# Performance work log

Measured on AMD Instinct MI355X. Metric: run time of the kernel, lower is better.

## Reference

```python
import jax, jax.numpy as jnp
import numpy as np

B, L, D, H = 8, 1024, 1024, 16
K = D // H

def setup_inputs() -> dict:
    key = jax.random.key(0)
    k1, k2, k3 = jax.random.split(key, 3)
    scale = 1.0 / np.sqrt(D)
    return {
        "x": jax.random.normal(k1, (B, L, D), dtype=jnp.float32),
        "w_in": jax.random.normal(k2, (D, 3 * D), dtype=jnp.float32) * scale,
        "b_in": jnp.zeros((3 * D,), dtype=jnp.float32),
        "w_out": jax.random.normal(k3, (D, D), dtype=jnp.float32) * scale,
        "b_out": jnp.zeros((D,), dtype=jnp.float32),
    }

def reference(x, w_in, b_in, w_out, b_out):
    # Fused QKV projection: [B, L, 3D]
    qkv = x @ w_in + b_in
    q, k, v = jnp.split(qkv, 3, axis=-1)
    # [B, L, D] -> [B, H, L, K]
    def to_heads(t):
        return t.reshape(B, L, H, K).transpose(0, 2, 1, 3)
    q, k, v = to_heads(q), to_heads(k), to_heads(v)
    # Full [B, H, L, L] score matrix (non-flash, as in source)
    logits = jnp.einsum('bhlk,bhmk->bhlm', q, k) / jnp.sqrt(jnp.float32(K))
    # NOTE: the source computes softmax but then (bug, reproduced faithfully)
    # uses the raw logits in the value contraction. causal_mask defaults False.
    out = jnp.einsum('bhlm,bhmk->bhlk', logits, v)
    out = out.transpose(0, 2, 1, 3).reshape(B, L, D)
    return out @ w_out + b_out
```

## Files before the change

### kernel.cpp

```cpp
#include <hip/hip_runtime.h>
#include <hip/hip_bf16.h>


typedef __attribute__((ext_vector_type(8))) short short8;
typedef __attribute__((ext_vector_type(4))) float f32x4;

static __device__ __forceinline__ short f2bf(float f) {
  __hip_bfloat16 h = __float2bfloat16(f);
  return __builtin_bit_cast(short, h);
}
static __device__ __forceinline__ float bf2f(short s) {
  unsigned int u = ((unsigned int)(unsigned short)s) << 16;
  return __builtin_bit_cast(float, u);
}

#define GLOAD16(src, dst)                                        \
  __builtin_amdgcn_global_load_lds(                              \
      (const __attribute__((address_space(1))) void*)(src),      \
      (__attribute__((address_space(3))) void*)(dst), 16, 0, 0)

__global__ __launch_bounds__(256) void cast_f32_bf16_kernel(
    const float* __restrict__ in, __hip_bfloat16* __restrict__ out) {
  size_t i = ((size_t)blockIdx.x * 256 + threadIdx.x) * 8;
  float4 v0 = *(const float4*)(in + i);
  float4 v1 = *(const float4*)(in + i + 4);
  short8 o;
  o[0] = f2bf(v0.x); o[1] = f2bf(v0.y); o[2] = f2bf(v0.z); o[3] = f2bf(v0.w);
  o[4] = f2bf(v1.x); o[5] = f2bf(v1.y); o[6] = f2bf(v1.z); o[7] = f2bf(v1.w);
  *(short8*)((__hip_bfloat16*)out + i) = o;
}

__global__ __launch_bounds__(256) void transpose_cast_kernel(
    const float* __restrict__ in, __hip_bfloat16* __restrict__ out, int R, int C) {
  __shared__ float tile[32][33];
  int c0 = blockIdx.x * 32, r0 = blockIdx.y * 32;
  int tx = threadIdx.x & 31;
  int ty = threadIdx.x >> 5;
#pragma unroll
  for (int i = 0; i < 4; ++i)
    tile[ty + i * 8][tx] = in[(size_t)(r0 + ty + i * 8) * C + c0 + tx];
  __syncthreads();
#pragma unroll
  for (int i = 0; i < 4; ++i)
    out[(size_t)(c0 + ty + i * 8) * R + r0 + tx] =
        __float2bfloat16(tile[tx][ty + i * 8]);
}

static __device__ __forceinline__ void store_out(__hip_bfloat16* p, float v) {
  *p = __float2bfloat16(v);
}
static __device__ __forceinline__ void store_out(float* p, float v) { *p = v; }

template <typename OutT, int KD, int AS, int NBN, int NOUT, long BTB>
__global__ __launch_bounds__(256) void gemm_bt_kernel(
    const __hip_bfloat16* __restrict__ A, const __hip_bfloat16* __restrict__ Bt,
    const float* __restrict__ bias, OutT* __restrict__ C) {
  __shared__ __align__(16) __hip_bfloat16 As[128 * 32];
  __shared__ __align__(16) __hip_bfloat16 Bs[128 * 32];

  const int t = threadIdx.x;
  A += (size_t)blockIdx.y * 1024 * AS;
  Bt += (size_t)blockIdx.y * BTB;
  C += (size_t)blockIdx.y * 1024 * NOUT;

  const int cpx = gridDim.x >> 3;
  const int wg = (blockIdx.x & 7) * cpx + (blockIdx.x >> 3);
  const int bm = wg / NBN, bn = wg % NBN;
  const int m0 = bm * 128, n0 = bn * 128;

  const int w = t >> 6, lane = t & 63;
  const int wr = w >> 1, wc = w & 1;
  const int lr = lane & 15, kg = lane >> 4;

  const int g0 = w * 128 + lane;
  const int g1 = g0 + 64;
  const __hip_bfloat16* srcA0 = A + (size_t)(m0 + (g0 >> 2)) * AS + (g0 & 3) * 8;
  const __hip_bfloat16* srcA1 = A + (size_t)(m0 + (g1 >> 2)) * AS + (g1 & 3) * 8;
  const __hip_bfloat16* srcB0 = Bt + (size_t)(n0 + (g0 >> 2)) * KD + (g0 & 3) * 8;
  const __hip_bfloat16* srcB1 = Bt + (size_t)(n0 + (g1 >> 2)) * KD + (g1 & 3) * 8;
  __hip_bfloat16* ldsA0 = As + (size_t)(w * 128) * 8;
  __hip_bfloat16* ldsA1 = As + (size_t)(w * 128 + 64) * 8;
  __hip_bfloat16* ldsB0 = Bs + (size_t)(w * 128) * 8;
  __hip_bfloat16* ldsB1 = Bs + (size_t)(w * 128 + 64) * 8;

  f32x4 acc[4][4] = {};

#pragma unroll 1
  for (int kt = 0; kt < KD / 32; ++kt) {
    GLOAD16(srcA0, ldsA0);
    GLOAD16(srcA1, ldsA1);
    GLOAD16(srcB0, ldsB0);
    GLOAD16(srcB1, ldsB1);
    srcA0 += 32; srcA1 += 32; srcB0 += 32; srcB1 += 32;
    __syncthreads();

    short8 af[4], bfv[4];
#pragma unroll
    for (int mi = 0; mi < 4; ++mi)
      af[mi] = *(const short8*)&As[(wr * 64 + mi * 16 + lr) * 32 + kg * 8];
#pragma unroll
    for (int ni = 0; ni < 4; ++ni)
      bfv[ni] = *(const short8*)&Bs[(wc * 64 + ni * 16 + lr) * 32 + kg * 8];
#pragma unroll
    for (int mi = 0; mi < 4; ++mi)
#pragma unroll
      for (int ni = 0; ni < 4; ++ni)
        acc[mi][ni] = __builtin_amdgcn_mfma_f32_16x16x32_bf16(
            af[mi], bfv[ni], acc[mi][ni], 0, 0, 0);
    __syncthreads();
  }

#pragma unroll
  for (int mi = 0; mi < 4; ++mi) {
    int row0 = m0 + wr * 64 + mi * 16 + kg * 4;
#pragma unroll
    for (int ni = 0; ni < 4; ++ni) {
      int col = n0 + wc * 64 + ni * 16 + lr;
      float bv = bias[col];
#pragma unroll
      for (int r = 0; r < 4; ++r)
        store_out(&C[(size_t)(row0 + r) * NOUT + col], acc[mi][ni][r] + bv);
    }
  }
}

__global__ __launch_bounds__(256) void ktv_kernel(
    const __hip_bfloat16* __restrict__ qkv, float* __restrict__ Spart) {
  __shared__ __align__(16) float Ks[64][68];
  __shared__ __align__(16) float Vs[64][68];
  const int bh = blockIdx.x;
  const int ch = blockIdx.y;
  const int b = bh >> 4, h = bh & 15;
  const __hip_bfloat16* base = qkv + (size_t)b * 1024 * 3072;
  const int hoff = h * 64;
  const int t = threadIdx.x;
  const int i0 = (t >> 4) * 4;
  const int j0 = (t & 15) * 4;
  const int srow = t >> 2;
  const int sg0 = t & 3;

  f32x4 acc[4] = {};

  for (int c = 0; c < 2; ++c) {
    int l0 = ch * 128 + c * 64;
#pragma unroll
    for (int rep = 0; rep < 2; ++rep) {
      int g = sg0 + rep * 4;
      const __hip_bfloat16* rowp = base + (size_t)(l0 + srow) * 3072;
      short8 kv = *(const short8*)(rowp + 1024 + hoff + g * 8);
      short8 vv = *(const short8*)(rowp + 2048 + hoff + g * 8);
      f32x4 k0, k1, v0, v1;
#pragma unroll
      for (int e = 0; e < 4; ++e) {
        k0[e] = bf2f(kv[e]); k1[e] = bf2f(kv[4 + e]);
        v0[e] = bf2f(vv[e]); v1[e] = bf2f(vv[4 + e]);
      }
      *(f32x4*)&Ks[srow][g * 8] = k0;
      *(f32x4*)&Ks[srow][g * 8 + 4] = k1;
      *(f32x4*)&Vs[srow][g * 8] = v0;
      *(f32x4*)&Vs[srow][g * 8 + 4] = v1;
    }
    __syncthreads();
#pragma unroll 8
    for (int l = 0; l < 64; ++l) {
      f32x4 kq = *(const f32x4*)&Ks[l][i0];
      f32x4 vq = *(const f32x4*)&Vs[l][j0];
#pragma unroll
      for (int ii = 0; ii < 4; ++ii) acc[ii] += kq[ii] * vq;
    }
    __syncthreads();
  }

  float* Sp = Spart + ((size_t)ch * 128 + bh) * 4096;
#pragma unroll
  for (int ii = 0; ii < 4; ++ii)
#pragma unroll
    for (int jj = 0; jj < 4; ++jj)
      Sp[(i0 + ii) * 64 + j0 + jj] = acc[ii][jj];
}

__global__ __launch_bounds__(512) void ut_kernel(
    const float* __restrict__ Spart, const __hip_bfloat16* __restrict__ w_outT,
    __hip_bfloat16* __restrict__ Ut) {
  __shared__ __align__(16) __hip_bfloat16 Sl[64][72];
  const int bh = blockIdx.x;
  const int b = bh >> 4, h = bh & 15;
  const int t = threadIdx.x, w = t >> 6, lane = t & 63;
  const int lr = lane & 15, kg = lane >> 4;

#pragma unroll
  for (int rep = 0; rep < 2; ++rep) {
    int e4 = t + rep * 512;
    int row = e4 >> 4, c4 = e4 & 15;
    f32x4 s = {};
#pragma unroll
    for (int c = 0; c < 8; ++c)
      s += *(const f32x4*)&Spart[((size_t)c * 128 + bh) * 4096 + row * 64 + c4 * 4];
    s *= 0.125f;
    __hip_bfloat16* p = &Sl[row][c4 * 4];
    p[0] = __float2bfloat16(s[0]); p[1] = __float2bfloat16(s[1]);
    p[2] = __float2bfloat16(s[2]); p[3] = __float2bfloat16(s[3]);
  }
  __syncthreads();

  const __hip_bfloat16* Ap = w_outT + (size_t)(w * 128 + lr) * 1024 + h * 64 + kg * 8;
  short8 bF[4][2];
#pragma unroll
  for (int ni = 0; ni < 4; ++ni)
#pragma unroll
    for (int kk = 0; kk < 2; ++kk)
      bF[ni][kk] = *(const short8*)&Sl[ni * 16 + lr][kk * 32 + kg * 8];

  f32x4 acc[8][4] = {};
#pragma unroll
  for (int mi = 0; mi < 8; ++mi) {
#pragma unroll
    for (int kk = 0; kk < 2; ++kk) {
      short8 aF = *(const short8*)(Ap + (size_t)mi * 16 * 1024 + kk * 32);
#pragma unroll
      for (int ni = 0; ni < 4; ++ni)
        acc[mi][ni] = __builtin_amdgcn_mfma_f32_16x16x32_bf16(
            aF, bF[ni][kk], acc[mi][ni], 0, 0, 0);
    }
  }

  __hip_bfloat16* Up = Ut + (size_t)b * 1024 * 1024;
#pragma unroll
  for (int mi = 0; mi < 8; ++mi) {
    int row0 = w * 128 + mi * 16 + kg * 4;
#pragma unroll
    for (int ni = 0; ni < 4; ++ni) {
      int col = h * 64 + ni * 16 + lr;
#pragma unroll
      for (int r = 0; r < 4; ++r)
        Up[(size_t)(row0 + r) * 1024 + col] = __float2bfloat16(acc[mi][ni][r]);
    }
  }
}

extern "C" void kernel_launch(void* const* d_in, const int* in_sizes, int n_in,
                              void* d_out, int out_size, void* d_ws, size_t ws_size,
                              hipStream_t stream) {
  const float* x = (const float*)d_in[0];
  const float* w_in = (const float*)d_in[1];
  const float* b_in = (const float*)d_in[2];
  const float* w_out = (const float*)d_in[3];
  const float* b_out = (const float*)d_in[4];
  float* out = (float*)d_out;

  char* ws = (char*)d_ws;
  __hip_bfloat16* x_bf = (__hip_bfloat16*)ws;   ws += (size_t)8192 * 1024 * 2;
  __hip_bfloat16* w_inT = (__hip_bfloat16*)ws;  ws += (size_t)3072 * 1024 * 2;
  __hip_bfloat16* w_outT = (__hip_bfloat16*)ws; ws += (size_t)1024 * 1024 * 2;
  __hip_bfloat16* qkv = (__hip_bfloat16*)ws;    ws += (size_t)8192 * 3072 * 2;
  float* Spart = (float*)ws;                    ws += (size_t)8 * 128 * 64 * 64 * 4;
  __hip_bfloat16* Ut = (__hip_bfloat16*)ws;     ws += (size_t)8 * 1024 * 1024 * 2;

  cast_f32_bf16_kernel<<<4096, 256, 0, stream>>>(x, x_bf);
  transpose_cast_kernel<<<dim3(96, 32), 256, 0, stream>>>(w_in, w_inT, 1024, 3072);
  transpose_cast_kernel<<<dim3(32, 32), 256, 0, stream>>>(w_out, w_outT, 1024, 1024);

  gemm_bt_kernel<__hip_bfloat16, 1024, 1024, 24, 3072, 0>
      <<<dim3(1536, 1), 256, 0, stream>>>(x_bf, w_inT, b_in, qkv);

  ktv_kernel<<<dim3(128, 8), 256, 0, stream>>>(qkv, Spart);

  ut_kernel<<<128, 512, 0, stream>>>(Spart, w_outT, Ut);

  gemm_bt_kernel<float, 1024, 3072, 8, 1024, 1024 * 1024>
      <<<dim3(64, 8), 256, 0, stream>>>(qkv, Ut, b_out, out);
}
```

Before: 156.0 us.

## Switch GEMM to 32x32x16 MFMA with K=64 tiles and fragment-ordered LDS layout

Rewrites the bf16 GEMM inner loop to use 32x32x16 MFMA instructions instead of 16x16x32, with each wave computing a 2x2 grid of 32x32 tiles. The K step per iteration doubles to 64, which halves the number of barrier pairs, and LDS is laid out in MFMA fragment order so each lane reads one contiguous short8 without bank conflicts. The intent is fewer LDS reads and syncs per FLOP and better MFMA throughput. The trade-off is more LDS use per block, and the epilogue has to remap accumulator rows to the 32x32 output layout.

Result: slower. 166.5 us (+6.7%).

```diff
diff --git a/kernel.cpp b/kernel.cpp
--- a/kernel.cpp
+++ b/kernel.cpp
@@ -4,6 +4,7 @@
 
 typedef __attribute__((ext_vector_type(8))) short short8;
 typedef __attribute__((ext_vector_type(4))) float f32x4;
+typedef __attribute__((ext_vector_type(16))) float f32x16;
 
 static __device__ __forceinline__ short f2bf(float f) {
   __hip_bfloat16 h = __float2bfloat16(f);
@@ -55,8 +56,8 @@
 __global__ __launch_bounds__(256) void gemm_bt_kernel(
     const __hip_bfloat16* __restrict__ A, const __hip_bfloat16* __restrict__ Bt,
     const float* __restrict__ bias, OutT* __restrict__ C) {
-  __shared__ __align__(16) __hip_bfloat16 As[128 * 32];
-  __shared__ __align__(16) __hip_bfloat16 Bs[128 * 32];
+  __shared__ short8 As[1024];
+  __shared__ short8 Bs[1024];
 
   const int t = threadIdx.x;
   A += (size_t)blockIdx.y * 1024 * AS;
@@ -70,58 +71,60 @@
 
   const int w = t >> 6, lane = t & 63;
   const int wr = w >> 1, wc = w & 1;
-  const int lr = lane & 15, kg = lane >> 4;
-
-  const int g0 = w * 128 + lane;
-  const int g1 = g0 + 64;
-  const __hip_bfloat16* srcA0 = A + (size_t)(m0 + (g0 >> 2)) * AS + (g0 & 3) * 8;
-  const __hip_bfloat16* srcA1 = A + (size_t)(m0 + (g1 >> 2)) * AS + (g1 & 3) * 8;
-  const __hip_bfloat16* srcB0 = Bt + (size_t)(n0 + (g0 >> 2)) * KD + (g0 & 3) * 8;
-  const __hip_bfloat16* srcB1 = Bt + (size_t)(n0 + (g1 >> 2)) * KD + (g1 & 3) * 8;
-  __hip_bfloat16* ldsA0 = As + (size_t)(w * 128) * 8;
-  __hip_bfloat16* ldsA1 = As + (size_t)(w * 128 + 64) * 8;
-  __hip_bfloat16* ldsB0 = Bs + (size_t)(w * 128) * 8;
-  __hip_bfloat16* ldsB1 = Bs + (size_t)(w * 128 + 64) * 8;
-
-  f32x4 acc[4][4] = {};
+  const int lr31 = lane & 31, hi = lane >> 5;
+
+  const __hip_bfloat16* srcA[4];
+  const __hip_bfloat16* srcB[4];
+#pragma unroll
+  for (int i = 0; i < 4; ++i) {
+    int p = w * 256 + i * 64 + lane;
+    int s = p >> 6, g = p & 63;
+    int row = (s >> 2) * 32 + (g >> 1);
+    int c = (s & 3) * 2 + (g & 1);
+    srcA[i] = A + (size_t)(m0 + row) * AS + c * 8;
+    srcB[i] = Bt + (size_t)(n0 + row) * KD + c * 8;
+  }
+
+  f32x16 acc[2][2] = {};
+  const int fo = lr31 * 2 + hi;
 
 #pragma unroll 1
-  for (int kt = 0; kt < KD / 32; ++kt) {
-    GLOAD16(srcA0, ldsA0);
-    GLOAD16(srcA1, ldsA1);
-    GLOAD16(srcB0, ldsB0);
-    GLOAD16(srcB1, ldsB1);
-    srcA0 += 32; srcA1 += 32; srcB0 += 32; srcB1 += 32;
-    __syncthreads();
-
-    short8 af[4], bfv[4];
-#pragma unroll
-    for (int mi = 0; mi < 4; ++mi)
-      af[mi] = *(const short8*)&As[(wr * 64 + mi * 16 + lr) * 32 + kg * 8];
-#pragma unroll
-    for (int ni = 0; ni < 4; ++ni)
-      bfv[ni] = *(const short8*)&Bs[(wc * 64 + ni * 16 + lr) * 32 + kg * 8];
-#pragma unroll
-    for (int mi = 0; mi < 4; ++mi)
-#pragma unroll
-      for (int ni = 0; ni < 4; ++ni)
-        acc[mi][ni] = __builtin_amdgcn_mfma_f32_16x16x32_bf16(
-            af[mi], bfv[ni], acc[mi][ni], 0, 0, 0);
-    __syncthreads();
-  }
-
-#pragma unroll
-  for (int mi = 0; mi < 4; ++mi) {
-    int row0 = m0 + wr * 64 + mi * 16 + kg * 4;
-#pragma unroll
-    for (int ni = 0; ni < 4; ++ni) {
-      int col = n0 + wc * 64 + ni * 16 + lr;
+  for (int kt = 0; kt < KD / 64; ++kt) {
+#pragma unroll
+    for (int i = 0; i < 4; ++i) {
+      GLOAD16(srcA[i], &As[w * 256 + i * 64]);
+      GLOAD16(srcB[i], &Bs[w * 256 + i * 64]);
+      srcA[i] += 64;
+      srcB[i] += 64;
+    }
+    __syncthreads();
+
+#pragma unroll
+    for (int ks = 0; ks < 4; ++ks) {
+      short8 a0 = As[((wr * 2 + 0) * 4 + ks) * 64 + fo];
+      short8 a1 = As[((wr * 2 + 1) * 4 + ks) * 64 + fo];
+      short8 b0 = Bs[((wc * 2 + 0) * 4 + ks) * 64 + fo];
+      short8 b1 = Bs[((wc * 2 + 1) * 4 + ks) * 64 + fo];
+      acc[0][0] = __builtin_amdgcn_mfma_f32_32x32x16_bf16(a0, b0, acc[0][0], 0, 0, 0);
+      acc[0][1] = __builtin_amdgcn_mfma_f32_32x32x16_bf16(a0, b1, acc[0][1], 0, 0, 0);
+      acc[1][0] = __builtin_amdgcn_mfma_f32_32x32x16_bf16(a1, b0, acc[1][0], 0, 0, 0);
+      acc[1][1] = __builtin_amdgcn_mfma_f32_32x32x16_bf16(a1, b1, acc[1][1], 0, 0, 0);
+    }
+    __syncthreads();
+  }
+
+#pragma unroll
+  for (int mi = 0; mi < 2; ++mi)
+#pragma unroll
+    for (int ni = 0; ni < 2; ++ni) {
+      int col = n0 + wc * 64 + ni * 32 + lr31;
       float bv = bias[col];
 #pragma unroll
-      for (int r = 0; r < 4; ++r)
-        store_out(&C[(size_t)(row0 + r) * NOUT + col], acc[mi][ni][r] + bv);
-    }
-  }
+      for (int r = 0; r < 16; ++r) {
+        int row = m0 + wr * 64 + mi * 32 + (r & 3) + 8 * (r >> 2) + 4 * hi;
+        store_out(&C[(size_t)row * NOUT + col], acc[mi][ni][r] + bv);
+      }
+    }
 }
 
 __global__ __launch_bounds__(256) void ktv_kernel(
```

## Double-buffer GEMM LDS tiles and merge prep casts into one kernel

Applied to the files above, without the earlier changes.

The GEMM now keeps two LDS buffers per operand and issues the global-to-LDS loads for the next K-step before computing on the current one, so load latency can overlap the MFMA work. The three prep kernels (x cast, w_in and w_out transpose-casts) are merged into a single launch that dispatches on block index, cutting launch overhead and letting the pieces run concurrently. Double buffering doubles LDS use per block, which may lower occupancy. There is also no explicit wait on the async loads before the barrier beyond the existing __syncthreads placement, so correctness relies on the barrier draining the outstanding loads.

Result: faster. 142.4 us (-8.8%).

```diff
diff --git a/kernel.cpp b/kernel.cpp
--- a/kernel.cpp
+++ b/kernel.cpp
@@ -19,21 +19,9 @@
       (const __attribute__((address_space(1))) void*)(src),      \
       (__attribute__((address_space(3))) void*)(dst), 16, 0, 0)
 
-__global__ __launch_bounds__(256) void cast_f32_bf16_kernel(
-    const float* __restrict__ in, __hip_bfloat16* __restrict__ out) {
-  size_t i = ((size_t)blockIdx.x * 256 + threadIdx.x) * 8;
-  float4 v0 = *(const float4*)(in + i);
-  float4 v1 = *(const float4*)(in + i + 4);
-  short8 o;
-  o[0] = f2bf(v0.x); o[1] = f2bf(v0.y); o[2] = f2bf(v0.z); o[3] = f2bf(v0.w);
-  o[4] = f2bf(v1.x); o[5] = f2bf(v1.y); o[6] = f2bf(v1.z); o[7] = f2bf(v1.w);
-  *(short8*)((__hip_bfloat16*)out + i) = o;
-}
-
-__global__ __launch_bounds__(256) void transpose_cast_kernel(
-    const float* __restrict__ in, __hip_bfloat16* __restrict__ out, int R, int C) {
-  __shared__ float tile[32][33];
-  int c0 = blockIdx.x * 32, r0 = blockIdx.y * 32;
+static __device__ __forceinline__ void transpose_body(
+    const float* __restrict__ in, __hip_bfloat16* __restrict__ out,
+    int R, int C, int c0, int r0, float tile[32][33]) {
   int tx = threadIdx.x & 31;
   int ty = threadIdx.x >> 5;
 #pragma unroll
@@ -44,6 +32,29 @@
   for (int i = 0; i < 4; ++i)
     out[(size_t)(c0 + ty + i * 8) * R + r0 + tx] =
         __float2bfloat16(tile[tx][ty + i * 8]);
+}
+
+__global__ __launch_bounds__(256) void prep_kernel(
+    const float* __restrict__ x, __hip_bfloat16* __restrict__ x_bf,
+    const float* __restrict__ w_in, __hip_bfloat16* __restrict__ w_inT,
+    const float* __restrict__ w_out, __hip_bfloat16* __restrict__ w_outT) {
+  __shared__ float tile[32][33];
+  const int bx = blockIdx.x;
+  if (bx < 4096) {
+    size_t i = ((size_t)bx * 256 + threadIdx.x) * 8;
+    float4 v0 = *(const float4*)(x + i);
+    float4 v1 = *(const float4*)(x + i + 4);
+    short8 o;
+    o[0] = f2bf(v0.x); o[1] = f2bf(v0.y); o[2] = f2bf(v0.z); o[3] = f2bf(v0.w);
+    o[4] = f2bf(v1.x); o[5] = f2bf(v1.y); o[6] = f2bf(v1.z); o[7] = f2bf(v1.w);
+    *(short8*)((__hip_bfloat16*)x_bf + i) = o;
+  } else if (bx < 4096 + 3072) {
+    int b = bx - 4096;
+    transpose_body(w_in, w_inT, 1024, 3072, (b % 96) * 32, (b / 96) * 32, tile);
+  } else {
+    int b = bx - 7168;
+    transpose_body(w_out, w_outT, 1024, 1024, (b % 32) * 32, (b / 32) * 32, tile);
+  }
 }
 
 static __device__ __forceinline__ void store_out(__hip_bfloat16* p, float v) {
@@ -55,8 +66,8 @@
 __global__ __launch_bounds__(256) void gemm_bt_kernel(
     const __hip_bfloat16* __restrict__ A, const __hip_bfloat16* __restrict__ Bt,
     const float* __restrict__ bias, OutT* __restrict__ C) {
-  __shared__ __align__(16) __hip_bfloat16 As[128 * 32];
-  __shared__ __align__(16) __hip_bfloat16 Bs[128 * 32];
+  __shared__ __align__(16) __hip_bfloat16 As[2][128 * 32];
+  __shared__ __align__(16) __hip_bfloat16 Bs[2][128 * 32];
 
   const int t = threadIdx.x;
   A += (size_t)blockIdx.y * 1024 * AS;
@@ -78,29 +89,37 @@
   const __hip_bfloat16* srcA1 = A + (size_t)(m0 + (g1 >> 2)) * AS + (g1 & 3) * 8;
   const __hip_bfloat16* srcB0 = Bt + (size_t)(n0 + (g0 >> 2)) * KD + (g0 & 3) * 8;
   const __hip_bfloat16* srcB1 = Bt + (size_t)(n0 + (g1 >> 2)) * KD + (g1 & 3) * 8;
-  __hip_bfloat16* ldsA0 = As + (size_t)(w * 128) * 8;
-  __hip_bfloat16* ldsA1 = As + (size_t)(w * 128 + 64) * 8;
-  __hip_bfloat16* ldsB0 = Bs + (size_t)(w * 128) * 8;
-  __hip_bfloat16* ldsB1 = Bs + (size_t)(w * 128 + 64) * 8;
+  const int lds0 = w * 128 * 8;
+  const int lds1 = (w * 128 + 64) * 8;
 
   f32x4 acc[4][4] = {};
-
+  constexpr int steps = KD / 32;
+
+  GLOAD16(srcA0, &As[0][lds0]);
+  GLOAD16(srcA1, &As[0][lds1]);
+  GLOAD16(srcB0, &Bs[0][lds0]);
+  GLOAD16(srcB1, &Bs[0][lds1]);
+  __syncthreads();
+
+  int cur = 0;
 #pragma unroll 1
-  for (int kt = 0; kt < KD / 32; ++kt) {
-    GLOAD16(srcA0, ldsA0);
-    GLOAD16(srcA1, ldsA1);
-    GLOAD16(srcB0, ldsB0);
-    GLOAD16(srcB1, ldsB1);
-    srcA0 += 32; srcA1 += 32; srcB0 += 32; srcB1 += 32;
-    __syncthreads();
-
+  for (int kt = 0; kt < steps; ++kt) {
+    if (kt + 1 < steps) {
+      const int ko = (kt + 1) * 32;
+      GLOAD16(srcA0 + ko, &As[cur ^ 1][lds0]);
+      GLOAD16(srcA1 + ko, &As[cur ^ 1][lds1]);
+      GLOAD16(srcB0 + ko, &Bs[cur ^ 1][lds0]);
+      GLOAD16(srcB1 + ko, &Bs[cur ^ 1][lds1]);
+    }
+    const __hip_bfloat16* Ac = As[cur];
+    const __hip_bfloat16* Bc = Bs[cur];
     short8 af[4], bfv[4];
 #pragma unroll
     for (int mi = 0; mi < 4; ++mi)
-      af[mi] = *(const short8*)&As[(wr * 64 + mi * 16 + lr) * 32 + kg * 8];
+      af[mi] = *(const short8*)&Ac[(wr * 64 + mi * 16 + lr) * 32 + kg * 8];
 #pragma unroll
     for (int ni = 0; ni < 4; ++ni)
-      bfv[ni] = *(const short8*)&Bs[(wc * 64 + ni * 16 + lr) * 32 + kg * 8];
+      bfv[ni] = *(const short8*)&Bc[(wc * 64 + ni * 16 + lr) * 32 + kg * 8];
 #pragma unroll
     for (int mi = 0; mi < 4; ++mi)
 #pragma unroll
@@ -108,6 +127,7 @@
         acc[mi][ni] = __builtin_amdgcn_mfma_f32_16x16x32_bf16(
             af[mi], bfv[ni], acc[mi][ni], 0, 0, 0);
     __syncthreads();
+    cur ^= 1;
   }
 
 #pragma unroll
@@ -256,9 +276,7 @@
   float* Spart = (float*)ws;                    ws += (size_t)8 * 128 * 64 * 64 * 4;
   __hip_bfloat16* Ut = (__hip_bfloat16*)ws;     ws += (size_t)8 * 1024 * 1024 * 2;
 
-  cast_f32_bf16_kernel<<<4096, 256, 0, stream>>>(x, x_bf);
-  transpose_cast_kernel<<<dim3(96, 32), 256, 0, stream>>>(w_in, w_inT, 1024, 3072);
-  transpose_cast_kernel<<<dim3(32, 32), 256, 0, stream>>>(w_out, w_outT, 1024, 1024);
+  prep_kernel<<<8192, 256, 0, stream>>>(x, x_bf, w_in, w_inT, w_out, w_outT);
 
   gemm_bt_kernel<__hip_bfloat16, 1024, 1024, 24, 3072, 0>
       <<<dim3(1536, 1), 256, 0, stream>>>(x_bf, w_inT, b_in, qkv);
```
